# Kernel optimization log

Hardware: AMD Instinct MI355X
Metric: run time of the kernel (lower is better)

The kernel has to match this reference:

```python
import jax, jax.numpy as jnp
import numpy as np

B, S, D, H = 2, 2048, 1024, 16
HD = D // H  # head_dim = 64
SCALE = HD ** -0.5


def setup_inputs() -> dict:
    key = jax.random.key(0)
    ks = jax.random.split(key, 10)
    std = D ** -0.5
    return {
        "x": jax.random.normal(ks[0], (B, S, D), jnp.float32),
        "y": jax.random.normal(ks[1], (B, S, D), jnp.float32),
        "Wq": jax.random.normal(ks[2], (D, D), jnp.float32) * std,
        "bq": jnp.zeros((D,), jnp.float32),
        "Wk": jax.random.normal(ks[3], (D, D), jnp.float32) * std,
        "bk": jnp.zeros((D,), jnp.float32),
        "Wv": jax.random.normal(ks[4], (D, D), jnp.float32) * std,
        "bv": jnp.zeros((D,), jnp.float32),
        "Wo": jax.random.normal(ks[5], (D, D), jnp.float32) * std,
        "bo": jnp.zeros((D,), jnp.float32),
    }


def reference(x, y, Wq, bq, Wk, bk, Wv, bv, Wo, bo):
    # Linear projections (torch Linear: x @ W.T + b; here W stored as [in,out])
    q = x @ Wq + bq  # [B,S,D]
    k = y @ Wk + bk
    v = y @ Wv + bv
    # split heads -> [B,H,S,hd]
    q = q.reshape(B, S, H, HD).transpose(0, 2, 1, 3)
    k = k.reshape(B, S, H, HD).transpose(0, 2, 1, 3)
    v = v.reshape(B, S, H, HD).transpose(0, 2, 1, 3)
    scores = jnp.einsum("bhqd,bhkd->bhqk", q, k) * SCALE  # [B,H,S,S]
    causal = jnp.tril(jnp.ones((S, S), dtype=bool))  # keep lower triangle
    scores = jnp.where(causal[None, None], scores, -jnp.inf)
    attn = jax.nn.softmax(scores, axis=-1)
    out = jnp.einsum("bhqk,bhkd->bhqd", attn, v)  # [B,H,S,hd]
    out = out.transpose(0, 2, 1, 3).reshape(B, S, D)
    return out @ Wo + bo
```

## Files before the change

### kernel.cpp

```cpp
#include <hip/hip_runtime.h>
#include <hip/hip_bf16.h>


#define BDIM 2
#define SDIM 2048
#define DDIM 1024
#define HDIM 16
#define HD   64
#define MDIM (BDIM*SDIM)
#define C2 0.18033688011112042f

using short8  = __attribute__((ext_vector_type(8))) short;
using floatx4 = __attribute__((ext_vector_type(4))) float;

static __device__ __forceinline__ unsigned short f2bf(float x) {
    union { float f; unsigned int u; } c; c.f = x;
    unsigned int r = (c.u + 0x7fffu + ((c.u >> 16) & 1u)) >> 16;
    return (unsigned short)r;
}

static __device__ __forceinline__ unsigned int pack2bf(float a, float b) {
    union { float f; unsigned int u; } ua, ub;
    ua.f = a; ub.f = b;
    return __builtin_amdgcn_perm(ub.u + 0x8000u, ua.u + 0x8000u, 0x07060302u);
}

#define GLD16(g, l) __builtin_amdgcn_global_load_lds(                        \
    (const __attribute__((address_space(1))) void*)(g),                      \
    (__attribute__((address_space(3))) void*)(l), 16, 0, 0)

__global__ __launch_bounds__(256) void cast_bf16_kernel(
    const float* __restrict__ X, const float* __restrict__ Y,
    unsigned short* __restrict__ Xo, unsigned short* __restrict__ Yo)
{
    const float* A    = blockIdx.z ? Y : X;
    unsigned short* O = blockIdx.z ? Yo : Xo;
    const int idx = blockIdx.x * 256 + threadIdx.x;
    const float4 a = ((const float4*)A)[idx*2];
    const float4 b = ((const float4*)A)[idx*2 + 1];
    ushort4 lo, hi;
    lo.x = f2bf(a.x); lo.y = f2bf(a.y); lo.z = f2bf(a.z); lo.w = f2bf(a.w);
    hi.x = f2bf(b.x); hi.y = f2bf(b.y); hi.z = f2bf(b.z); hi.w = f2bf(b.w);
    ((ushort4*)O)[idx*2]     = lo;
    ((ushort4*)O)[idx*2 + 1] = hi;
}

__global__ __launch_bounds__(256) void wtrans_kernel(
    const float* __restrict__ W0, const float* __restrict__ W1,
    const float* __restrict__ W2, const float* __restrict__ W3,
    unsigned short* __restrict__ T0, unsigned short* __restrict__ T1,
    unsigned short* __restrict__ T2, unsigned short* __restrict__ T3)
{
    __shared__ float tile[64][68];
    const int z = blockIdx.z;
    const float* W    = (z == 0) ? W0 : (z == 1) ? W1 : (z == 2) ? W2 : W3;
    unsigned short* T = (z == 0) ? T0 : (z == 1) ? T1 : (z == 2) ? T2 : T3;
    const int k0 = blockIdx.x * 64, n0 = blockIdx.y * 64;
    const int t = threadIdx.x;
    #pragma unroll
    for (int i = 0; i < 4; ++i) {
        const int idx = t + i*256;
        const int kr = idx >> 4, c4 = idx & 15;
        float4 v = *(const float4*)&W[(size_t)(k0 + kr) * DDIM + n0 + c4*4];
        tile[kr][c4*4+0] = v.x; tile[kr][c4*4+1] = v.y;
        tile[kr][c4*4+2] = v.z; tile[kr][c4*4+3] = v.w;
    }
    __syncthreads();
    #pragma unroll
    for (int i = 0; i < 4; ++i) {
        const int idx = t + i*256;
        const int nr = idx >> 4, kc = idx & 15;
        ushort4 o;
        o.x = f2bf(tile[kc*4+0][nr]); o.y = f2bf(tile[kc*4+1][nr]);
        o.z = f2bf(tile[kc*4+2][nr]); o.w = f2bf(tile[kc*4+3][nr]);
        *(ushort4*)&T[(size_t)(n0 + nr) * DDIM + k0 + kc*4] = o;
    }
}

__device__ __forceinline__ void gemm128_core(
    const unsigned short* __restrict__ A, const unsigned short* __restrict__ Bt,
    int bm, int bn, unsigned short* As, unsigned short* Bs, floatx4 acc[4][4])
{
    const int t = threadIdx.x;
    const int w = t >> 6, l = t & 63;
    const int quad = l >> 4, col = l & 15;
    const int wr = (w >> 1) * 64, wc = (w & 1) * 64;

    const int c1 = t + 256;
    const int r0 = t >> 2,  o0 = (t & 3) * 8;
    const int r1 = c1 >> 2, o1 = (c1 & 3) * 8;

    const unsigned short* Ar0 = A  + (size_t)(bm + r0) * DDIM + o0;
    const unsigned short* Ar1 = A  + (size_t)(bm + r1) * DDIM + o1;
    const unsigned short* Br0 = Bt + (size_t)(bn + r0) * DDIM + o0;
    const unsigned short* Br1 = Bt + (size_t)(bn + r1) * DDIM + o1;

    for (int kt = 0; kt < DDIM; kt += 32) {
        __syncthreads();
        GLD16(Ar0 + kt, As + t*8);
        GLD16(Ar1 + kt, As + c1*8);
        GLD16(Br0 + kt, Bs + t*8);
        GLD16(Br1 + kt, Bs + c1*8);
        __syncthreads();
        short8 af[4], bfr[4];
        #pragma unroll
        for (int i = 0; i < 4; ++i)
            af[i] = *(const short8*)&As[(wr + i*16 + col)*32 + quad*8];
        #pragma unroll
        for (int j = 0; j < 4; ++j)
            bfr[j] = *(const short8*)&Bs[(wc + j*16 + col)*32 + quad*8];
        #pragma unroll
        for (int i = 0; i < 4; ++i)
            #pragma unroll
            for (int j = 0; j < 4; ++j)
                acc[i][j] = __builtin_amdgcn_mfma_f32_16x16x32_bf16(
                    af[i], bfr[j], acc[i][j], 0, 0, 0);
    }
}

__global__ __launch_bounds__(256) void qkv_gemm_kernel(
    const unsigned short* __restrict__ xbf, const unsigned short* __restrict__ ybf,
    const unsigned short* __restrict__ Wqt, const unsigned short* __restrict__ Wkt,
    const unsigned short* __restrict__ Wvt,
    const float* __restrict__ bq, const float* __restrict__ bk,
    const float* __restrict__ bv,
    unsigned short* __restrict__ Qbf, unsigned short* __restrict__ Kbf,
    unsigned short* __restrict__ vT)
{
    __shared__ __align__(16) unsigned short As[128*32];
    __shared__ __align__(16) unsigned short Bs[128*32];

    const int z = blockIdx.z;
    const unsigned short* A  = (z == 0) ? xbf : ybf;
    const unsigned short* Wt = (z == 0) ? Wqt : (z == 1) ? Wkt : Wvt;
    const float* bp          = (z == 0) ? bq  : (z == 1) ? bk  : bv;

    const int bm = blockIdx.y * 128, bn = blockIdx.x * 128;
    floatx4 acc[4][4] = {};
    gemm128_core(A, Wt, bm, bn, As, Bs, acc);

    const int t = threadIdx.x;
    const int w = t >> 6, l = t & 63;
    const int quad = l >> 4, col = l & 15;
    const int wr = (w >> 1) * 64, wc = (w & 1) * 64;

    #pragma unroll
    for (int j = 0; j < 4; ++j) {
        const int gn = bn + wc + j*16 + col;
        const float bias = bp[gn];
        #pragma unroll
        for (int i = 0; i < 4; ++i) {
            const int gm0 = bm + wr + i*16 + quad*4;
            if (z == 0) {
                #pragma unroll
                for (int r = 0; r < 4; ++r)
                    Qbf[(size_t)(gm0 + r) * DDIM + gn] = f2bf((acc[i][j][r] + bias) * C2);
            } else if (z == 1) {
                #pragma unroll
                for (int r = 0; r < 4; ++r)
                    Kbf[(size_t)(gm0 + r) * DDIM + gn] = f2bf(acc[i][j][r] + bias);
            } else {
                ushort4 o;
                o.x = f2bf(acc[i][j][0] + bias); o.y = f2bf(acc[i][j][1] + bias);
                o.z = f2bf(acc[i][j][2] + bias); o.w = f2bf(acc[i][j][3] + bias);
                *(ushort4*)&vT[((size_t)((gm0 >> 11) * DDIM + gn)) * SDIM + (gm0 & 2047)] = o;
            }
        }
    }
}

__global__ __launch_bounds__(256) void out_gemm_kernel(
    const unsigned short* __restrict__ Obf, const unsigned short* __restrict__ Wot,
    const float* __restrict__ bo, float* __restrict__ out)
{
    __shared__ __align__(16) unsigned short As[128*32];
    __shared__ __align__(16) unsigned short Bs[128*32];

    const int bm = blockIdx.y * 128, bn = blockIdx.x * 128;
    floatx4 acc[4][4] = {};
    gemm128_core(Obf, Wot, bm, bn, As, Bs, acc);

    const int t = threadIdx.x;
    const int w = t >> 6, l = t & 63;
    const int quad = l >> 4, col = l & 15;
    const int wr = (w >> 1) * 64, wc = (w & 1) * 64;

    #pragma unroll
    for (int j = 0; j < 4; ++j) {
        const int gn = bn + wc + j*16 + col;
        const float bias = bo[gn];
        #pragma unroll
        for (int i = 0; i < 4; ++i) {
            const int gm0 = bm + wr + i*16 + quad*4;
            #pragma unroll
            for (int r = 0; r < 4; ++r)
                out[(size_t)(gm0 + r) * DDIM + gn] = acc[i][j][r] + bias;
        }
    }
}

__global__ __launch_bounds__(128) void attn_mfma_kernel(
    const unsigned short* __restrict__ Qbf, const unsigned short* __restrict__ Kbf,
    const unsigned short* __restrict__ vT, unsigned short* __restrict__ Obf)
{
    __shared__ __align__(16) unsigned short KfL[2][512*8];
    __shared__ __align__(16) unsigned short VfL[2][512*8];
    __shared__ __align__(16) unsigned short PfL[4*1024];

    const int t = threadIdx.x;
    const int w = t >> 6, l = t & 63;
    const int quad = l >> 4, col = l & 15;
    const int jt = blockIdx.x;
    const int h  = blockIdx.y, b = blockIdx.z;
    const size_t hoff = (size_t)h * HD;
    const size_t bS = (size_t)b * SDIM;
    const size_t bD = (size_t)b * DDIM;

    const unsigned short* kp[4];
    const unsigned short* vp[4];
    #pragma unroll
    for (int i = 0; i < 4; ++i) {
        kp[i] = Kbf + (bS + i*16 + col) * DDIM + hoff + w*32 + quad*8;
        vp[i] = vT  + (bD + hoff + i*16 + col) * SDIM + w*32 + quad*8;
    }

    #pragma unroll 1
    for (int ph = 0; ph < 2; ++ph) {
        const int qt  = ph ? (31 - jt) : jt;
        const int qb  = qt * 64;
        const int qwb = qb + w * 32;
        const int nk  = qt + 1;

        short8 qf[2][2];
        #pragma unroll
        for (int qs = 0; qs < 2; ++qs)
            #pragma unroll
            for (int kc = 0; kc < 2; ++kc)
                qf[qs][kc] = *(const short8*)
                    &Qbf[(bS + qwb + qs*16 + col) * DDIM + hoff + kc*32 + quad*8];

        float lrun[2] = {0.0f, 0.0f};
        floatx4 o[2][4] = {};

        __syncthreads();
        #pragma unroll
        for (int i = 0; i < 4; ++i) {
            GLD16(kp[i], &KfL[0][((i*2 + w)*64 + l)*8]);
            GLD16(vp[i], &VfL[0][((i*2 + w)*64 + l)*8]);
        }

        #pragma unroll 1
        for (int it = 0; it < nk; ++it) {
            const int ktb = it * 64;
            const int cur = it & 1;
            __syncthreads();
            if (it + 1 < nk) {
                const int nxt = cur ^ 1;
                const size_t ko = (size_t)(it + 1) * 64 * DDIM;
                const int    vo = (it + 1) * 64;
                #pragma unroll
                for (int i = 0; i < 4; ++i) {
                    GLD16(kp[i] + ko, &KfL[nxt][((i*2 + w)*64 + l)*8]);
                    GLD16(vp[i] + vo, &VfL[nxt][((i*2 + w)*64 + l)*8]);
                }
            }
            if (ktb > qwb + 31) continue;

            const unsigned short* Kb = KfL[cur];
            const unsigned short* Vb = VfL[cur];
            short8 kf[4][2], vfr[4][2];
            #pragma unroll
            for (int kt = 0; kt < 4; ++kt)
                #pragma unroll
                for (int kc = 0; kc < 2; ++kc)
                    kf[kt][kc] = *(const short8*)&Kb[((kt*2 + kc)*64 + l)*8];
            #pragma unroll
            for (int n = 0; n < 4; ++n)
                #pragma unroll
                for (int kk = 0; kk < 2; ++kk)
                    vfr[n][kk] = *(const short8*)&Vb[((n*2 + kk)*64 + l)*8];

            #pragma unroll
            for (int qs = 0; qs < 2; ++qs) {
                if (ktb > qwb + qs*16 + 15) continue;

                floatx4 sT[4];
                #pragma unroll
                for (int kt = 0; kt < 4; ++kt) {
                    floatx4 z = {};
                    z = __builtin_amdgcn_mfma_f32_16x16x32_bf16(kf[kt][0], qf[qs][0], z, 0, 0, 0);
                    z = __builtin_amdgcn_mfma_f32_16x16x32_bf16(kf[kt][1], qf[qs][1], z, 0, 0, 0);
                    sT[kt] = z;
                }

                const int qrow = qwb + qs*16 + col;
                const bool anymask = (ktb + 63 > qwb + qs*16);
                float p[4][4];
                #pragma unroll
                for (int kt = 0; kt < 4; ++kt)
                    #pragma unroll
                    for (int r = 0; r < 4; ++r) {
                        float xv = sT[kt][r];
                        if (anymask && (ktb + kt*16 + quad*4 + r > qrow))
                            xv = -1e30f;
                        p[kt][r] = exp2f(xv);
                    }

                float st[4];
                #pragma unroll
                for (int kt = 0; kt < 4; ++kt)
                    st[kt] = (p[kt][0] + p[kt][1]) + (p[kt][2] + p[kt][3]);
                lrun[qs] += (st[0] + st[1]) + (st[2] + st[3]);

                const int pb = (w*2 + qs) * 1024;
                #pragma unroll
                for (int kt = 0; kt < 4; ++kt) {
                    uint2 pk;
                    pk.x = pack2bf(p[kt][0], p[kt][1]);
                    pk.y = pack2bf(p[kt][2], p[kt][3]);
                    *(uint2*)&PfL[pb + ((kt*2 + (quad>>1))*16 + col)*8 + (quad&1)*4] = pk;
                }
                const short8 pf0 = *(const short8*)&PfL[pb + ((0*4 + quad)*16 + col)*8];
                const short8 pf1 = *(const short8*)&PfL[pb + ((1*4 + quad)*16 + col)*8];
                #pragma unroll
                for (int n = 0; n < 4; ++n) {
                    o[qs][n] = __builtin_amdgcn_mfma_f32_16x16x32_bf16(vfr[n][0], pf0, o[qs][n], 0, 0, 0);
                    o[qs][n] = __builtin_amdgcn_mfma_f32_16x16x32_bf16(vfr[n][1], pf1, o[qs][n], 0, 0, 0);
                }
            }
        }

        #pragma unroll
        for (int qs = 0; qs < 2; ++qs) {
            float lt = lrun[qs];
            lt += __shfl_xor(lt, 16);
            lt += __shfl_xor(lt, 32);
            const float inv = 1.0f / lt;
            #pragma unroll
            for (int n = 0; n < 4; ++n) {
                ushort4 pk;
                pk.x = f2bf(o[qs][n][0] * inv); pk.y = f2bf(o[qs][n][1] * inv);
                pk.z = f2bf(o[qs][n][2] * inv); pk.w = f2bf(o[qs][n][3] * inv);
                *(ushort4*)&Obf[(bS + qwb + qs*16 + col) * DDIM + hoff + n*16 + quad*4] = pk;
            }
        }
    }
}

extern "C" void kernel_launch(void* const* d_in, const int* in_sizes, int n_in,
                              void* d_out, int out_size, void* d_ws, size_t ws_size,
                              hipStream_t stream) {
    const float* x  = (const float*)d_in[0];
    const float* y  = (const float*)d_in[1];
    const float* Wq = (const float*)d_in[2];
    const float* bq = (const float*)d_in[3];
    const float* Wk = (const float*)d_in[4];
    const float* bk = (const float*)d_in[5];
    const float* Wv = (const float*)d_in[6];
    const float* bv = (const float*)d_in[7];
    const float* Wo = (const float*)d_in[8];
    const float* bo = (const float*)d_in[9];
    float* out = (float*)d_out;

    const size_t mat  = (size_t)MDIM * DDIM;
    const size_t wmat = (size_t)DDIM * DDIM;
    unsigned short* p = (unsigned short*)d_ws;
    unsigned short* xbf = p;            p += mat;
    unsigned short* ybf = p;            p += mat;
    unsigned short* Wqt = p;            p += wmat;
    unsigned short* Wkt = p;            p += wmat;
    unsigned short* Wvt = p;            p += wmat;
    unsigned short* Wot = p;            p += wmat;
    unsigned short* Qbf = p;            p += mat;
    unsigned short* Kbf = p;            p += mat;
    unsigned short* vT  = p;            p += mat;
    unsigned short* Obf = p;            p += mat;

    hipLaunchKernelGGL(cast_bf16_kernel, dim3(MDIM*DDIM/8/256, 1, 2), dim3(256),
                       0, stream, x, y, xbf, ybf);
    hipLaunchKernelGGL(wtrans_kernel, dim3(16, 16, 4), dim3(256), 0, stream,
                       Wq, Wk, Wv, Wo, Wqt, Wkt, Wvt, Wot);

    hipLaunchKernelGGL(qkv_gemm_kernel, dim3(DDIM/128, MDIM/128, 3), dim3(256),
                       0, stream, xbf, ybf, Wqt, Wkt, Wvt, bq, bk, bv,
                       Qbf, Kbf, vT);

    hipLaunchKernelGGL(attn_mfma_kernel, dim3(16, HDIM, BDIM), dim3(128),
                       0, stream, Qbf, Kbf, vT, Obf);

    hipLaunchKernelGGL(out_gemm_kernel, dim3(DDIM/128, MDIM/128), dim3(256),
                       0, stream, Obf, Wot, bo, out);
}
```

Measured before the change: 254.5 us.

## Run both paired causal query tiles concurrently in one 256-thread block

```diff
diff --git a/kernel.cpp b/kernel.cpp
--- a/kernel.cpp
+++ b/kernel.cpp
@@ -199,13 +199,13 @@
     }
 }
 
-__global__ __launch_bounds__(128) void attn_mfma_kernel(
+__global__ __launch_bounds__(256) void attn_mfma_kernel(
     const unsigned short* __restrict__ Qbf, const unsigned short* __restrict__ Kbf,
     const unsigned short* __restrict__ vT, unsigned short* __restrict__ Obf)
 {
     __shared__ __align__(16) unsigned short KfL[2][512*8];
     __shared__ __align__(16) unsigned short VfL[2][512*8];
-    __shared__ __align__(16) unsigned short PfL[4*1024];
+    __shared__ __align__(16) unsigned short PfL[8*1024];
 
     const int t = threadIdx.x;
     const int w = t >> 6, l = t & 63;
@@ -216,133 +216,133 @@
     const size_t bS = (size_t)b * SDIM;
     const size_t bD = (size_t)b * DDIM;
 
-    const unsigned short* kp[4];
-    const unsigned short* vp[4];
-    #pragma unroll
-    for (int i = 0; i < 4; ++i) {
-        kp[i] = Kbf + (bS + i*16 + col) * DDIM + hoff + w*32 + quad*8;
-        vp[i] = vT  + (bD + hoff + i*16 + col) * SDIM + w*32 + quad*8;
+    const int qt  = (w < 2) ? jt : (31 - jt);
+    const int qwb = qt * 64 + (w & 1) * 32;
+    const int nk_wave  = qt + 1;
+    const int nk_block = 32 - jt;
+
+    const unsigned short* kp[2];
+    const unsigned short* vp[2];
+    int kdst[2], vdst[2];
+    #pragma unroll
+    for (int i = 0; i < 2; ++i) {
+        const int f = 2*w + i;
+        kp[i]   = Kbf + (bS + (f >> 1)*16 + col) * DDIM + hoff + (f & 1)*32 + quad*8;
+        vp[i]   = vT  + (bD + hoff + (f >> 1)*16 + col) * SDIM + (f & 1)*32 + quad*8;
+        kdst[i] = (f*64 + l)*8;
+        vdst[i] = (f*64 + l)*8;
+    }
+
+    short8 qf[2][2];
+    #pragma unroll
+    for (int qs = 0; qs < 2; ++qs)
+        #pragma unroll
+        for (int kc = 0; kc < 2; ++kc)
+            qf[qs][kc] = *(const short8*)
+                &Qbf[(bS + qwb + qs*16 + col) * DDIM + hoff + kc*32 + quad*8];
+
+    float lrun[2] = {0.0f, 0.0f};
+    floatx4 o[2][4] = {};
+
+    #pragma unroll
+    for (int i = 0; i < 2; ++i) {
+        GLD16(kp[i], &KfL[0][kdst[i]]);
+        GLD16(vp[i], &VfL[0][vdst[i]]);
     }
 
     #pragma unroll 1
-    for (int ph = 0; ph < 2; ++ph) {
-        const int qt  = ph ? (31 - jt) : jt;
-        const int qb  = qt * 64;
-        const int qwb = qb + w * 32;
-        const int nk  = qt + 1;
-
-        short8 qf[2][2];
-        #pragma unroll
-        for (int qs = 0; qs < 2; ++qs)
+    for (int it = 0; it < nk_block; ++it) {
+        const int ktb = it * 64;
+        const int cur = it & 1;
+        __syncthreads();
+        if (it + 1 < nk_block) {
+            const int nxt = cur ^ 1;
+            const size_t ko = (size_t)(it + 1) * 64 * DDIM;
+            const int    vo = (it + 1) * 64;
+            #pragma unroll
+            for (int i = 0; i < 2; ++i) {
+                GLD16(kp[i] + ko, &KfL[nxt][kdst[i]]);
+                GLD16(vp[i] + vo, &VfL[nxt][vdst[i]]);
+            }
+        }
+        if (it >= nk_wave) continue;
+
+        const unsigned short* Kb = KfL[cur];
+        const unsigned short* Vb = VfL[cur];
+        short8 kf[4][2], vfr[4][2];
+        #pragma unroll
+        for (int kt = 0; kt < 4; ++kt)
             #pragma unroll
             for (int kc = 0; kc < 2; ++kc)
-                qf[qs][kc] = *(const short8*)
-                    &Qbf[(bS + qwb + qs*16 + col) * DDIM + hoff + kc*32 + quad*8];
-
-        float lrun[2] = {0.0f, 0.0f};
-        floatx4 o[2][4] = {};
-
-        __syncthreads();
-        #pragma unroll
-        for (int i = 0; i < 4; ++i) {
-            GLD16(kp[i], &KfL[0][((i*2 + w)*64 + l)*8]);
-            GLD16(vp[i], &VfL[0][((i*2 + w)*64 + l)*8]);
-        }
-
-        #pragma unroll 1
-        for (int it = 0; it < nk; ++it) {
-            const int ktb = it * 64;
-            const int cur = it & 1;
-            __syncthreads();
-            if (it + 1 < nk) {
-                const int nxt = cur ^ 1;
-                const size_t ko = (size_t)(it + 1) * 64 * DDIM;
-                const int    vo = (it + 1) * 64;
-                #pragma unroll
-                for (int i = 0; i < 4; ++i) {
-                    GLD16(kp[i] + ko, &KfL[nxt][((i*2 + w)*64 + l)*8]);
-                    GLD16(vp[i] + vo, &VfL[nxt][((i*2 + w)*64 + l)*8]);
-                }
-            }
-            if (ktb > qwb + 31) continue;
-
-            const unsigned short* Kb = KfL[cur];
-            const unsigned short* Vb = VfL[cur];
-            short8 kf[4][2], vfr[4][2];
+                kf[kt][kc] = *(const short8*)&Kb[((kt*2 + kc)*64 + l)*8];
+        #pragma unroll
+        for (int n = 0; n < 4; ++n)
+            #pragma unroll
+            for (int kk = 0; kk < 2; ++kk)
+                vfr[n][kk] = *(const short8*)&Vb[((n*2 + kk)*64 + l)*8];
+
+        #pragma unroll
+        for (int qs = 0; qs < 2; ++qs) {
+            if (ktb > qwb + qs*16 + 15) continue;
+
+            floatx4 sT[4];
+            #pragma unroll
+            for (int kt = 0; kt < 4; ++kt) {
+                floatx4 z = {};
+                z = __builtin_amdgcn_mfma_f32_16x16x32_bf16(kf[kt][0], qf[qs][0], z, 0, 0, 0);
+                z = __builtin_amdgcn_mfma_f32_16x16x32_bf16(kf[kt][1], qf[qs][1], z, 0, 0, 0);
+                sT[kt] = z;
+            }
+
+            const int qrow = qwb + qs*16 + col;
+            const bool anymask = (ktb + 63 > qwb + qs*16);
+            float p[4][4];
             #pragma unroll
             for (int kt = 0; kt < 4; ++kt)
                 #pragma unroll
-                for (int kc = 0; kc < 2; ++kc)
-                    kf[kt][kc] = *(const short8*)&Kb[((kt*2 + kc)*64 + l)*8];
-            #pragma unroll
-            for (int n = 0; n < 4; ++n)
-                #pragma unroll
-                for (int kk = 0; kk < 2; ++kk)
-                    vfr[n][kk] = *(const short8*)&Vb[((n*2 + kk)*64 + l)*8];
-
-            #pragma unroll
-            for (int qs = 0; qs < 2; ++qs) {
-                if (ktb > qwb + qs*16 + 15) continue;
-
-                floatx4 sT[4];
-                #pragma unroll
-                for (int kt = 0; kt < 4; ++kt) {
-                    floatx4 z = {};
-                    z = __builtin_amdgcn_mfma_f32_16x16x32_bf16(kf[kt][0], qf[qs][0], z, 0, 0, 0);
-                    z = __builtin_amdgcn_mfma_f32_16x16x32_bf16(kf[kt][1], qf[qs][1], z, 0, 0, 0);
-                    sT[kt] = z;
+                for (int r = 0; r < 4; ++r) {
+                    float xv = sT[kt][r];
+                    if (anymask && (ktb + kt*16 + quad*4 + r > qrow))
+                        xv = -1e30f;
+                    p[kt][r] = exp2f(xv);
                 }
 
-                const int qrow = qwb + qs*16 + col;
-                const bool anymask = (ktb + 63 > qwb + qs*16);
-                float p[4][4];
-                #pragma unroll
-                for (int kt = 0; kt < 4; ++kt)
-                    #pragma unroll
-                    for (int r = 0; r < 4; ++r) {
-                        float xv = sT[kt][r];
-                        if (anymask && (ktb + kt*16 + quad*4 + r > qrow))
-                            xv = -1e30f;
-                        p[kt][r] = exp2f(xv);
-                    }
-
-                float st[4];
-                #pragma unroll
-                for (int kt = 0; kt < 4; ++kt)
-                    st[kt] = (p[kt][0] + p[kt][1]) + (p[kt][2] + p[kt][3]);
-                lrun[qs] += (st[0] + st[1]) + (st[2] + st[3]);
-
-                const int pb = (w*2 + qs) * 1024;
-                #pragma unroll
-                for (int kt = 0; kt < 4; ++kt) {
-                    uint2 pk;
-                    pk.x = pack2bf(p[kt][0], p[kt][1]);
-                    pk.y = pack2bf(p[kt][2], p[kt][3]);
-                    *(uint2*)&PfL[pb + ((kt*2 + (quad>>1))*16 + col)*8 + (quad&1)*4] = pk;
-                }
-                const short8 pf0 = *(const short8*)&PfL[pb + ((0*4 + quad)*16 + col)*8];
-                const short8 pf1 = *(const short8*)&PfL[pb + ((1*4 + quad)*16 + col)*8];
-                #pragma unroll
-                for (int n = 0; n < 4; ++n) {
-                    o[qs][n] = __builtin_amdgcn_mfma_f32_16x16x32_bf16(vfr[n][0], pf0, o[qs][n], 0, 0, 0);
-                    o[qs][n] = __builtin_amdgcn_mfma_f32_16x16x32_bf16(vfr[n][1], pf1, o[qs][n], 0, 0, 0);
-                }
-            }
-        }
-
-        #pragma unroll
-        for (int qs = 0; qs < 2; ++qs) {
-            float lt = lrun[qs];
-            lt += __shfl_xor(lt, 16);
-            lt += __shfl_xor(lt, 32);
-            const float inv = 1.0f / lt;
+            float st[4];
+            #pragma unroll
+            for (int kt = 0; kt < 4; ++kt)
+                st[kt] = (p[kt][0] + p[kt][1]) + (p[kt][2] + p[kt][3]);
+            lrun[qs] += (st[0] + st[1]) + (st[2] + st[3]);
+
+            const int pb = (w*2 + qs) * 1024;
+            #pragma unroll
+            for (int kt = 0; kt < 4; ++kt) {
+                uint2 pk;
+                pk.x = pack2bf(p[kt][0], p[kt][1]);
+                pk.y = pack2bf(p[kt][2], p[kt][3]);
+                *(uint2*)&PfL[pb + ((kt*2 + (quad>>1))*16 + col)*8 + (quad&1)*4] = pk;
+            }
+            const short8 pf0 = *(const short8*)&PfL[pb + ((0*4 + quad)*16 + col)*8];
+            const short8 pf1 = *(const short8*)&PfL[pb + ((1*4 + quad)*16 + col)*8];
             #pragma unroll
             for (int n = 0; n < 4; ++n) {
-                ushort4 pk;
-                pk.x = f2bf(o[qs][n][0] * inv); pk.y = f2bf(o[qs][n][1] * inv);
-                pk.z = f2bf(o[qs][n][2] * inv); pk.w = f2bf(o[qs][n][3] * inv);
-                *(ushort4*)&Obf[(bS + qwb + qs*16 + col) * DDIM + hoff + n*16 + quad*4] = pk;
-            }
+                o[qs][n] = __builtin_amdgcn_mfma_f32_16x16x32_bf16(vfr[n][0], pf0, o[qs][n], 0, 0, 0);
+                o[qs][n] = __builtin_amdgcn_mfma_f32_16x16x32_bf16(vfr[n][1], pf1, o[qs][n], 0, 0, 0);
+            }
+        }
+    }
+
+    #pragma unroll
+    for (int qs = 0; qs < 2; ++qs) {
+        float lt = lrun[qs];
+        lt += __shfl_xor(lt, 16);
+        lt += __shfl_xor(lt, 32);
+        const float inv = 1.0f / lt;
+        #pragma unroll
+        for (int n = 0; n < 4; ++n) {
+            ushort4 pk;
+            pk.x = f2bf(o[qs][n][0] * inv); pk.y = f2bf(o[qs][n][1] * inv);
+            pk.z = f2bf(o[qs][n][2] * inv); pk.w = f2bf(o[qs][n][3] * inv);
+            *(ushort4*)&Obf[(bS + qwb + qs*16 + col) * DDIM + hoff + n*16 + quad*4] = pk;
         }
     }
 }
@@ -385,7 +385,7 @@
                        0, stream, xbf, ybf, Wqt, Wkt, Wvt, bq, bk, bv,
                        Qbf, Kbf, vT);
 
-    hipLaunchKernelGGL(attn_mfma_kernel, dim3(16, HDIM, BDIM), dim3(128),
+    hipLaunchKernelGGL(attn_mfma_kernel, dim3(16, HDIM, BDIM), dim3(256),
                        0, stream, Qbf, Kbf, vT, Obf);
 
     hipLaunchKernelGGL(out_gemm_kernel, dim3(DDIM/128, MDIM/128), dim3(256),
```

Result: faster. 245.7 us (-3.5%).
